# Kernel optimization log

Measured on AMD Instinct MI355X. Metric: run time of the kernel, lower is better.

## Reference

```python
import jax, jax.numpy as jnp
import numpy as np

B, C, IMG, P, D, L, NH, DFF = 8, 2, 256, 16, 1024, 8, 16, 4096
HP = IMG // P          # 16 patches per side
N = HP * HP            # 256 patch tokens
S = N + 1              # + cls token
HD = D // NH           # 64 head dim


def _ln(x, w, b, eps=1e-5):
    mu = x.mean(-1, keepdims=True)
    var = ((x - mu) ** 2).mean(-1, keepdims=True)
    return (x - mu) * jax.lax.rsqrt(var + eps) * w + b


def _decay_mask():
    # RetNetRelPos2d(D, NH, initial_value=1, heads_range=NH): per-head log-decay
    decay = jnp.log(1.0 - 2.0 ** (-1.0 - NH * jnp.arange(NH, dtype=jnp.float32) / NH))
    idx = jnp.arange(HP)
    gy, gx = jnp.meshgrid(idx, idx, indexing='ij')
    grid = jnp.stack([gy.ravel(), gx.ravel()], -1)                 # [N,2]
    dist = jnp.abs(grid[:, None] - grid[None, :]).sum(-1)          # [N,N] Manhattan
    mask = decay[:, None, None] * dist.astype(jnp.float32)        # [NH,N,N]
    return jnp.pad(mask, ((0, 0), (1, 0), (1, 0)))                 # cls: zero decay


def setup_inputs() -> dict:
    key = jax.random.key(0)
    ks = iter(jax.random.split(key, 16))
    g = lambda shape: jax.random.normal(next(ks), shape, jnp.float32) * 0.02
    return dict(
        imgs=jax.random.normal(next(ks), (B, C, IMG, IMG), jnp.float32),
        patch_w=g((C, P, P, D)), patch_b=jnp.zeros((D,), jnp.float32),
        cls_tok=g((1, 1, D)),
        ln1_w=jnp.ones((L, D), jnp.float32), ln1_b=jnp.zeros((L, D), jnp.float32),
        wq=g((L, D, D)), wk=g((L, D, D)), wv=g((L, D, D)),
        bq=jnp.zeros((L, D), jnp.float32), bk=jnp.zeros((L, D), jnp.float32), bv=jnp.zeros((L, D), jnp.float32),
        wo=g((L, D, D)), bo=jnp.zeros((L, D), jnp.float32),
        ln2_w=jnp.ones((L, D), jnp.float32), ln2_b=jnp.zeros((L, D), jnp.float32),
        w1=g((L, D, DFF)), b1=jnp.zeros((L, DFF), jnp.float32),
        w2=g((L, DFF, D)), b2=jnp.zeros((L, D), jnp.float32),
        normf_w=jnp.ones((D,), jnp.float32), normf_b=jnp.zeros((D,), jnp.float32),
        enpred_w=g((D, P * P * 2)), enpred_b=jnp.zeros((P * P * 2,), jnp.float32),
    )


def reference(imgs, patch_w, patch_b, cls_tok, ln1_w, ln1_b, wq, wk, wv, bq, bk, bv,
              wo, bo, ln2_w, ln2_b, w1, b1, w2, b2, normf_w, normf_b, enpred_w, enpred_b):
    b = imgs.shape[0]
    # PatchEmbed: conv with stride==kernel == patch extraction + linear
    xp = imgs.reshape(b, C, HP, P, HP, P)
    x = jnp.einsum('nchpwq,cpqd->nhwd', xp, patch_w).reshape(b, N, D) + patch_b
    residual = x
    x = jnp.concatenate([jnp.broadcast_to(cls_tok, (b, 1, D)), x], axis=1)  # [b,S,D]
    mask = _decay_mask()  # [NH,S,S]
    scale = HD ** -0.5
    for i in range(L):  # RMT blocks: pre-LN MaSA (softmax(qk*scale + decay)) + pre-LN GELU MLP
        h = _ln(x, ln1_w[i], ln1_b[i])
        q = (h @ wq[i] + bq[i]).reshape(b, S, NH, HD)
        k = (h @ wk[i] + bk[i]).reshape(b, S, NH, HD)
        v = (h @ wv[i] + bv[i]).reshape(b, S, NH, HD)
        logits = jnp.einsum('bqhd,bkhd->bhqk', q, k) * scale + mask
        attn = jax.nn.softmax(logits, axis=-1)
        o = jnp.einsum('bhqk,bkhd->bqhd', attn, v).reshape(b, S, D)
        x = x + o @ wo[i] + bo[i]
        h = _ln(x, ln2_w[i], ln2_b[i])
        x = x + jax.nn.gelu(h @ w1[i] + b1[i], approximate=False) @ w2[i] + b2[i]
    x = _ln(x, normf_w, normf_b)
    # PGSA on patch tokens as [b,D,HP,HP]
    t = x[:, 1:, :].transpose(0, 2, 1).reshape(b, D, HP, HP)
    n = HP * HP - 1
    mu = t.mean(axis=(2, 3), keepdims=True)
    xm2 = (t - mu) ** 2
    y = xm2 / (4.0 * (xm2.sum(axis=(2, 3), keepdims=True) / n + 1e-4)) + 0.5
    t = t * jax.nn.sigmoid(y)
    tokens = t.reshape(b, D, N).transpose(0, 2, 1) + residual
    pred = tokens @ enpred_w + enpred_b  # [b,N,P*P*2]
    # unpatchify -> [b,2,IMG,IMG]
    u = pred.reshape(b, HP, HP, P, P, 2)
    return jnp.einsum('nhwpqc->nchpwq', u).reshape(b, 2, IMG, IMG)
```

## Files before the change

kernel.cpp:

```cpp
#include <hip/hip_runtime.h>
#include <cstdint>
#include <cstddef>

#define BB    8
#define CCH   2
#define IMGD  256
#define PDIM  16
#define DD    1024
#define LLAY  8
#define NHEAD 16
#define DFFD  4096
#define NTOK  256
#define SD    257
#define HDD   64
#define MTOK  (BB*SD)
#define MPAT  (BB*NTOK)
#define MPAD  2176
#define KPAD  288

typedef unsigned short u16;
typedef __bf16 bf16x8 __attribute__((ext_vector_type(8)));
typedef float  f32x4  __attribute__((ext_vector_type(4)));

__device__ __forceinline__ u16 f2bf(float f) {
    uint32_t u = __float_as_uint(f);
    u += 0x7FFF + ((u >> 16) & 1);
    return (u16)(u >> 16);
}
__device__ __forceinline__ int imin(int a, int b) { return a < b ? a : b; }

#define GLB(p)  ((const __attribute__((address_space(1))) void*)(uintptr_t)(p))
#define LDSP(p) ((__attribute__((address_space(3))) void*)(uint32_t)(uintptr_t)(p))

template<int ACT, int OBF>
__global__ __launch_bounds__(256) void gemm128(
    const u16* __restrict__ A, const u16* __restrict__ BT,
    const float* __restrict__ bias, const float* __restrict__ Cin,
    void* __restrict__ Cout, int M, int N, int K)
{
    __shared__ u16 lds[8192];
    const int tid = threadIdx.x, wid = tid >> 6, lane = tid & 63;
    const int m0 = blockIdx.y * 128, n0 = blockIdx.x * 128;
    const int wm = (wid >> 1) * 64, wn = (wid & 1) * 64;
    const int srow = lane >> 2, scol = (lane & 3) * 8;
    const int l15 = lane & 15, loct = lane >> 4;

    f32x4 acc[4][4] = {};

    const size_t arow = (size_t)(m0 + wid * 16 + srow) * K + scol;
    const size_t brow = (size_t)(n0 + wid * 16 + srow) * K + scol;
    u16* ldsA = lds + wid * 512;
    u16* ldsB = lds + 4096 + wid * 512;

    for (int k0 = 0; k0 < K; k0 += 32) {
        __builtin_amdgcn_global_load_lds(GLB(A  + arow + k0),                 LDSP(ldsA),        16, 0, 0);
        __builtin_amdgcn_global_load_lds(GLB(A  + arow + (size_t)64*K + k0),  LDSP(ldsA + 2048), 16, 0, 0);
        __builtin_amdgcn_global_load_lds(GLB(BT + brow + k0),                 LDSP(ldsB),        16, 0, 0);
        __builtin_amdgcn_global_load_lds(GLB(BT + brow + (size_t)64*K + k0),  LDSP(ldsB + 2048), 16, 0, 0);
        __syncthreads();
        bf16x8 af[4], bfr[4];
        #pragma unroll
        for (int i = 0; i < 4; ++i)
            af[i] = *(const bf16x8*)(lds + (wm + i * 16 + l15) * 32 + loct * 8);
        #pragma unroll
        for (int j = 0; j < 4; ++j)
            bfr[j] = *(const bf16x8*)(lds + 4096 + (wn + j * 16 + l15) * 32 + loct * 8);
        #pragma unroll
        for (int i = 0; i < 4; ++i)
            #pragma unroll
            for (int j = 0; j < 4; ++j)
                acc[i][j] = __builtin_amdgcn_mfma_f32_16x16x32_bf16(af[i], bfr[j], acc[i][j], 0, 0, 0);
        __syncthreads();
    }

    #pragma unroll
    for (int j = 0; j < 4; ++j) {
        const int col = n0 + wn + j * 16 + l15;
        const float bv = bias[col];
        #pragma unroll
        for (int i = 0; i < 4; ++i) {
            const int rbase = m0 + wm + i * 16 + loct * 4;
            #pragma unroll
            for (int r = 0; r < 4; ++r) {
                const int row = rbase + r;
                if (row < M) {
                    float v = acc[i][j][r] + bv;
                    if (ACT) v = 0.5f * v * (1.f + erff(v * 0.70710678118654752f));
                    if (Cin) v += Cin[(size_t)row * N + col];
                    if (OBF) ((u16*)Cout)[(size_t)row * N + col] = f2bf(v);
                    else     ((float*)Cout)[(size_t)row * N + col] = v;
                }
            }
        }
    }
}

__global__ __launch_bounds__(256) void gemm_qkv(
    const u16* __restrict__ A, const u16* __restrict__ BT,
    const float* __restrict__ bias,
    u16* __restrict__ QKb, u16* __restrict__ VTg, int M, int K)
{
    __shared__ u16 lds[8192];
    const int tid = threadIdx.x, wid = tid >> 6, lane = tid & 63;
    const int m0 = blockIdx.y * 128, n0 = blockIdx.x * 128;
    const int wm = (wid >> 1) * 64, wn = (wid & 1) * 64;
    const int srow = lane >> 2, scol = (lane & 3) * 8;
    const int l15 = lane & 15, loct = lane >> 4;

    f32x4 acc[4][4] = {};
    const size_t arow = (size_t)(m0 + wid * 16 + srow) * K + scol;
    const size_t brow = (size_t)(n0 + wid * 16 + srow) * K + scol;
    u16* ldsA = lds + wid * 512;
    u16* ldsB = lds + 4096 + wid * 512;

    for (int k0 = 0; k0 < K; k0 += 32) {
        __builtin_amdgcn_global_load_lds(GLB(A  + arow + k0),                 LDSP(ldsA),        16, 0, 0);
        __builtin_amdgcn_global_load_lds(GLB(A  + arow + (size_t)64*K + k0),  LDSP(ldsA + 2048), 16, 0, 0);
        __builtin_amdgcn_global_load_lds(GLB(BT + brow + k0),                 LDSP(ldsB),        16, 0, 0);
        __builtin_amdgcn_global_load_lds(GLB(BT + brow + (size_t)64*K + k0),  LDSP(ldsB + 2048), 16, 0, 0);
        __syncthreads();
        bf16x8 af[4], bfr[4];
        #pragma unroll
        for (int i = 0; i < 4; ++i)
            af[i] = *(const bf16x8*)(lds + (wm + i * 16 + l15) * 32 + loct * 8);
        #pragma unroll
        for (int j = 0; j < 4; ++j)
            bfr[j] = *(const bf16x8*)(lds + 4096 + (wn + j * 16 + l15) * 32 + loct * 8);
        #pragma unroll
        for (int i = 0; i < 4; ++i)
            #pragma unroll
            for (int j = 0; j < 4; ++j)
                acc[i][j] = __builtin_amdgcn_mfma_f32_16x16x32_bf16(af[i], bfr[j], acc[i][j], 0, 0, 0);
        __syncthreads();
    }

    #pragma unroll
    for (int j = 0; j < 4; ++j) {
        const int col = n0 + wn + j * 16 + l15;
        const float bv = bias[col];
        #pragma unroll
        for (int i = 0; i < 4; ++i) {
            const int rbase = m0 + wm + i * 16 + loct * 4;
            #pragma unroll
            for (int r = 0; r < 4; ++r) {
                const int row = rbase + r;
                if (row < M) {
                    const float v = acc[i][j][r] + bv;
                    if (col < 2048) {
                        QKb[(size_t)row * 2048 + col] = f2bf(v);
                    } else {
                        const int b = row / SD;
                        const int key = row - b * SD;
                        VTg[((size_t)b * 1024 + (col - 2048)) * KPAD + key] = f2bf(v);
                    }
                }
            }
        }
    }
}

template<int ACT, int OBF>
__global__ __launch_bounds__(256) void gemm64(
    const u16* __restrict__ A, const u16* __restrict__ BT,
    const float* __restrict__ bias, const float* __restrict__ Cin,
    void* __restrict__ Cout, int M, int N, int K)
{
    __shared__ u16 lds[8192];
    const int tid = threadIdx.x, wid = tid >> 6, lane = tid & 63;
    const int m0 = blockIdx.y * 64, n0 = blockIdx.x * 64;
    const int wm = (wid >> 1) * 32, wn = (wid & 1) * 32;
    const int srow = lane >> 2, scol = (lane & 3) * 8;
    const int l15 = lane & 15, loct = lane >> 4;

    f32x4 acc[2][2] = {};
    const size_t arow = (size_t)(m0 + wid * 16 + srow) * K + scol;
    const size_t brow = (size_t)(n0 + wid * 16 + srow) * K + scol;
    u16* ldsA = lds + wid * 512;
    u16* ldsB = lds + 4096 + wid * 512;

    for (int k0 = 0; k0 < K; k0 += 64) {
        __builtin_amdgcn_global_load_lds(GLB(A  + arow + k0),      LDSP(ldsA),        16, 0, 0);
        __builtin_amdgcn_global_load_lds(GLB(A  + arow + k0 + 32), LDSP(ldsA + 2048), 16, 0, 0);
        __builtin_amdgcn_global_load_lds(GLB(BT + brow + k0),      LDSP(ldsB),        16, 0, 0);
        __builtin_amdgcn_global_load_lds(GLB(BT + brow + k0 + 32), LDSP(ldsB + 2048), 16, 0, 0);
        __syncthreads();
        #pragma unroll
        for (int t = 0; t < 2; ++t) {
            bf16x8 af[2], bfr[2];
            #pragma unroll
            for (int i = 0; i < 2; ++i)
                af[i] = *(const bf16x8*)(lds + t * 2048 + (wm + i * 16 + l15) * 32 + loct * 8);
            #pragma unroll
            for (int j = 0; j < 2; ++j)
                bfr[j] = *(const bf16x8*)(lds + 4096 + t * 2048 + (wn + j * 16 + l15) * 32 + loct * 8);
            #pragma unroll
            for (int i = 0; i < 2; ++i)
                #pragma unroll
                for (int j = 0; j < 2; ++j)
                    acc[i][j] = __builtin_amdgcn_mfma_f32_16x16x32_bf16(af[i], bfr[j], acc[i][j], 0, 0, 0);
        }
        __syncthreads();
    }

    #pragma unroll
    for (int j = 0; j < 2; ++j) {
        const int col = n0 + wn + j * 16 + l15;
        const float bv = bias[col];
        #pragma unroll
        for (int i = 0; i < 2; ++i) {
            const int rbase = m0 + wm + i * 16 + loct * 4;
            #pragma unroll
            for (int r = 0; r < 4; ++r) {
                const int row = rbase + r;
                if (row < M) {
                    float v = acc[i][j][r] + bv;
                    if (ACT) v = 0.5f * v * (1.f + erff(v * 0.70710678118654752f));
                    if (Cin) v += Cin[(size_t)row * N + col];
                    if (OBF) ((u16*)Cout)[(size_t)row * N + col] = f2bf(v);
                    else     ((float*)Cout)[(size_t)row * N + col] = v;
                }
            }
        }
    }
}

__global__ __launch_bounds__(256) void attn_fused(
    const u16* __restrict__ QKb, const u16* __restrict__ VTg,
    u16* __restrict__ O)
{
    __shared__ u16 P[4][16][296];
    const int tid = threadIdx.x, wid = tid >> 6, lane = tid & 63;
    const int l15 = lane & 15, loct = lane >> 4;
    const int bh = blockIdx.x, b = bh >> 4, h = bh & 15;
    const int q0 = blockIdx.y * 64 + wid * 16;

    const size_t qkbase = (size_t)b * SD * 2048 + h * 64;
    const u16* qp = QKb + qkbase + (size_t)imin(q0 + l15, SD - 1) * 2048;
    const bf16x8 qf0 = *(const bf16x8*)(qp + loct * 8);
    const bf16x8 qf1 = *(const bf16x8*)(qp + 32 + loct * 8);

    f32x4 s[17];
    #pragma unroll
    for (int nt = 0; nt < 17; ++nt) {
        const u16* kp = QKb + qkbase + (size_t)imin(nt * 16 + l15, SD - 1) * 2048 + 1024;
        const bf16x8 kf0 = *(const bf16x8*)(kp + loct * 8);
        const bf16x8 kf1 = *(const bf16x8*)(kp + 32 + loct * 8);
        f32x4 a = {};
        a = __builtin_amdgcn_mfma_f32_16x16x32_bf16(qf0, kf0, a, 0, 0, 0);
        a = __builtin_amdgcn_mfma_f32_16x16x32_bf16(qf1, kf1, a, 0, 0, 0);
        s[nt] = a;
    }

    const float dec = logf(1.f - exp2f(-1.f - (float)h));
    const int qb = q0 + loct * 4;
    float rmax[4] = {-3.4e38f, -3.4e38f, -3.4e38f, -3.4e38f};
    #pragma unroll
    for (int nt = 0; nt < 17; ++nt) {
        const int key = nt * 16 + l15;
        #pragma unroll
        for (int r = 0; r < 4; ++r) {
            float v;
            if (key >= SD) {
                v = -1e30f;
            } else {
                v = s[nt][r] * 0.125f;
                const int q = qb + r;
                if (q > 0 && key > 0) {
                    const int nq = q - 1, nk = key - 1;
                    const int dist = abs((nq >> 4) - (nk >> 4)) + abs((nq & 15) - (nk & 15));
                    v += dec * (float)dist;
                }
            }
            s[nt][r] = v;
            rmax[r] = fmaxf(rmax[r], v);
        }
    }
    #pragma unroll
    for (int r = 0; r < 4; ++r) {
        #pragma unroll
        for (int m = 1; m < 16; m <<= 1) rmax[r] = fmaxf(rmax[r], __shfl_xor(rmax[r], m));
    }
    float rsum[4] = {0.f, 0.f, 0.f, 0.f};
    #pragma unroll
    for (int nt = 0; nt < 17; ++nt)
        #pragma unroll
        for (int r = 0; r < 4; ++r) {
            const float e = __expf(s[nt][r] - rmax[r]);
            s[nt][r] = e;
            rsum[r] += e;
        }
    #pragma unroll
    for (int r = 0; r < 4; ++r) {
        #pragma unroll
        for (int m = 1; m < 16; m <<= 1) rsum[r] += __shfl_xor(rsum[r], m);
        rsum[r] = 1.f / rsum[r];
    }
    #pragma unroll
    for (int nt = 0; nt < 17; ++nt)
        #pragma unroll
        for (int r = 0; r < 4; ++r)
            P[wid][loct * 4 + r][nt * 16 + l15] = f2bf(s[nt][r] * rsum[r]);
    {
        const int rr = lane >> 2, cc = (lane & 3) * 4;
        #pragma unroll
        for (int i = 0; i < 4; ++i) P[wid][rr][272 + cc + i] = 0;
    }

    f32x4 o[4] = {};
    const u16* vrow = VTg + ((size_t)b * 1024 + h * 64) * KPAD;
    #pragma unroll
    for (int ks = 0; ks < 9; ++ks) {
        const bf16x8 pf = *(const bf16x8*)&P[wid][l15][ks * 32 + loct * 8];
        #pragma unroll
        for (int j = 0; j < 4; ++j) {
            const bf16x8 vf = *(const bf16x8*)(vrow + (size_t)(j * 16 + l15) * KPAD + ks * 32 + loct * 8);
            o[j] = __builtin_amdgcn_mfma_f32_16x16x32_bf16(pf, vf, o[j], 0, 0, 0);
        }
    }
    #pragma unroll
    for (int j = 0; j < 4; ++j)
        #pragma unroll
        for (int r = 0; r < 4; ++r) {
            const int q = qb + r;
            if (q < SD) O[((size_t)(b * SD + q)) * DD + h * 64 + j * 16 + l15] = f2bf(o[j][r]);
        }
}

__global__ __launch_bounds__(256) void transpose_bf16_k(
    const float* __restrict__ W, u16* __restrict__ WT, int K, int N)
{
    __shared__ float t[32][33];
    const int k0 = blockIdx.y * 32, n0 = blockIdx.x * 32;
    const int c = threadIdx.x & 31, rb = threadIdx.x >> 5;
    #pragma unroll
    for (int i = 0; i < 4; ++i) {
        const int r = rb + i * 8;
        t[r][c] = W[(size_t)(k0 + r) * N + n0 + c];
    }
    __syncthreads();
    #pragma unroll
    for (int i = 0; i < 4; ++i) {
        const int r = rb + i * 8;
        WT[(size_t)(n0 + r) * K + k0 + c] = f2bf(t[c][r]);
    }
}

__global__ __launch_bounds__(256) void cat3_k(const float* __restrict__ a,
                                              const float* __restrict__ b,
                                              const float* __restrict__ c,
                                              float* __restrict__ o)
{
    const int i = blockIdx.x * 256 + threadIdx.x;
    o[i] = (i < 1024) ? a[i] : (i < 2048 ? b[i - 1024] : c[i - 2048]);
}

__global__ __launch_bounds__(256) void im2col_k(const float* __restrict__ imgs,
                                                u16* __restrict__ Ao)
{
    const int idx = blockIdx.x * 256 + threadIdx.x;
    const int k = idx & 511, m = idx >> 9;
    const int b = m >> 8, n = m & 255;
    const int hp = n >> 4, wp = n & 15;
    const int c = k >> 8, p = (k >> 4) & 15, q = k & 15;
    Ao[idx] = f2bf(imgs[(((size_t)b * CCH + c) * IMGD + hp * PDIM + p) * IMGD + wp * PDIM + q]);
}

__global__ __launch_bounds__(256) void build_x_k(const float* __restrict__ RES,
                                                 const float* __restrict__ cls,
                                                 float* __restrict__ X)
{
    const int idx = blockIdx.x * 256 + threadIdx.x;
    const int d = idx & 1023;
    const int r = idx >> 10;
    const int b = r / SD;
    const int s = r - b * SD;
    X[idx] = (s == 0) ? cls[d] : RES[((size_t)(b * NTOK + s - 1)) * DD + d];
}

template<int OBF>
__global__ __launch_bounds__(256) void ln_rows(const float* __restrict__ X,
                                               const float* __restrict__ w,
                                               const float* __restrict__ bsrc,
                                               void* __restrict__ Y)
{
    const int row = blockIdx.x;
    const int tid = threadIdx.x;
    const float* xr = X + (size_t)row * DD;
    const float4 v = *(const float4*)(xr + tid * 4);
    float s  = v.x + v.y + v.z + v.w;
    float s2 = v.x * v.x + v.y * v.y + v.z * v.z + v.w * v.w;
    #pragma unroll
    for (int off = 1; off < 64; off <<= 1) {
        s  += __shfl_xor(s, off);
        s2 += __shfl_xor(s2, off);
    }
    __shared__ float rs[4], rs2[4];
    if ((tid & 63) == 0) { rs[tid >> 6] = s; rs2[tid >> 6] = s2; }
    __syncthreads();
    s  = rs[0] + rs[1] + rs[2] + rs[3];
    s2 = rs2[0] + rs2[1] + rs2[2] + rs2[3];
    const float mu  = s * (1.f / 1024.f);
    const float var = fmaf(-mu, mu, s2 * (1.f / 1024.f));
    const float ri  = rsqrtf(var + 1e-5f);
    const float4 wv = *(const float4*)(w + tid * 4);
    const float4 bv = *(const float4*)(bsrc + tid * 4);
    float4 o;
    o.x = (v.x - mu) * ri * wv.x + bv.x;
    o.y = (v.y - mu) * ri * wv.y + bv.y;
    o.z = (v.z - mu) * ri * wv.z + bv.z;
    o.w = (v.w - mu) * ri * wv.w + bv.w;
    if (OBF) {
        ushort4 o4 = make_ushort4(f2bf(o.x), f2bf(o.y), f2bf(o.z), f2bf(o.w));
        *(ushort4*)((u16*)Y + (size_t)row * DD + tid * 4) = o4;
    } else {
        *(float4*)((float*)Y + (size_t)row * DD + tid * 4) = o;
    }
}

__global__ __launch_bounds__(256) void pgsa_k(const float* __restrict__ Xf,
                                              const float* __restrict__ RES,
                                              u16* __restrict__ TOK)
{
    const int bd = blockIdx.x;
    const int b = bd >> 10, dch = bd & 1023;
    const int n = threadIdx.x;
    const float t = Xf[((size_t)(b * SD + 1 + n)) * DD + dch];
    __shared__ float red[4];
    float s = t;
    #pragma unroll
    for (int off = 1; off < 64; off <<= 1) s += __shfl_xor(s, off);
    if ((n & 63) == 0) red[n >> 6] = s;
    __syncthreads();
    const float mu = (red[0] + red[1] + red[2] + red[3]) * (1.f / 256.f);
    const float xm = t - mu;
    const float xm2 = xm * xm;
    __syncthreads();
    float s2 = xm2;
    #pragma unroll
    for (int off = 1; off < 64; off <<= 1) s2 += __shfl_xor(s2, off);
    if ((n & 63) == 0) red[n >> 6] = s2;
    __syncthreads();
    const float tot2 = red[0] + red[1] + red[2] + red[3];
    const float y = xm2 / (4.f * (tot2 * (1.f / 255.f) + 1e-4f)) + 0.5f;
    const float sig = 1.f / (1.f + expf(-y));
    const size_t ri = ((size_t)b * NTOK + n) * DD + dch;
    TOK[ri] = f2bf(fmaf(t, sig, RES[ri]));
}

__global__ __launch_bounds__(256) void unpatch_k(const float* __restrict__ PRED,
                                                 float* __restrict__ out)
{
    const int idx = blockIdx.x * 256 + threadIdx.x;
    const int j = idx & 255, i = (idx >> 8) & 255;
    const int c = (idx >> 16) & 1, b = idx >> 17;
    const int hp = i >> 4, p = i & 15, wp = j >> 4, q = j & 15;
    out[idx] = PRED[((size_t)b * NTOK + hp * 16 + wp) * 512 + (p * 16 + q) * 2 + c];
}

extern "C" void kernel_launch(void* const* d_in, const int* in_sizes, int n_in,
                              void* d_out, int out_size, void* d_ws, size_t ws_size,
                              hipStream_t stream)
{
    const float* imgs     = (const float*)d_in[0];
    const float* patch_w  = (const float*)d_in[1];
    const float* patch_b  = (const float*)d_in[2];
    const float* cls_tok  = (const float*)d_in[3];
    const float* ln1_w    = (const float*)d_in[4];
    const float* ln1_b    = (const float*)d_in[5];
    const float* wq       = (const float*)d_in[6];
    const float* wk       = (const float*)d_in[7];
    const float* wv       = (const float*)d_in[8];
    const float* bq       = (const float*)d_in[9];
    const float* bk       = (const float*)d_in[10];
    const float* bv       = (const float*)d_in[11];
    const float* wo       = (const float*)d_in[12];
    const float* bo       = (const float*)d_in[13];
    const float* ln2_w    = (const float*)d_in[14];
    const float* ln2_b    = (const float*)d_in[15];
    const float* w1       = (const float*)d_in[16];
    const float* b1       = (const float*)d_in[17];
    const float* w2       = (const float*)d_in[18];
    const float* b2       = (const float*)d_in[19];
    const float* normf_w  = (const float*)d_in[20];
    const float* normf_b  = (const float*)d_in[21];
    const float* enpred_w = (const float*)d_in[22];
    const float* enpred_b = (const float*)d_in[23];
    float* out = (float*)d_out;

    char* w = (char*)d_ws;
    float* X     = (float*)w;            w += (size_t)MTOK * DD * 4;
    float* RES   = (float*)w;            w += (size_t)MPAT * DD * 4;
    u16*   QKb   = (u16*)w;              w += (size_t)MPAD * 2048 * 2;
    u16*   VTg   = (u16*)w;              w += (size_t)BB * 1024 * KPAD * 2;
    char*  UNION = w;                    w += (size_t)MPAD * DFFD * 2;
    u16*   Hb    = (u16*)w;              w += (size_t)MPAD * DD * 2;
    u16*   Ob    = (u16*)w;              w += (size_t)MPAD * DD * 2;
    u16*   WT    = (u16*)w;              w += (size_t)DFFD * DD * 2;
    float* bias3 = (float*)w;            w += 3072 * 4;

    u16*   IM2b  = (u16*)UNION;
    u16*   GELUb = (u16*)UNION;
    float* PRED  = (float*)UNION;
    float* Hf    = (float*)QKb;
    u16*   TOKb  = Hb;

    hipMemsetAsync(VTg, 0, (size_t)BB * 1024 * KPAD * 2, stream);

    hipLaunchKernelGGL(im2col_k, dim3(4096), dim3(256), 0, stream, imgs, IM2b);
    hipLaunchKernelGGL(transpose_bf16_k, dim3(DD / 32, 512 / 32), dim3(256), 0, stream,
                       patch_w, WT, 512, DD);
    hipLaunchKernelGGL((gemm64<0,0>), dim3(DD / 64, MPAT / 64), dim3(256), 0, stream,
                       IM2b, WT, patch_b, (const float*)nullptr, (void*)RES, MPAT, DD, 512);
    hipLaunchKernelGGL(build_x_k, dim3(MTOK * DD / 256), dim3(256), 0, stream, RES, cls_tok, X);

    for (int i = 0; i < LLAY; ++i) {
        const size_t wOff = (size_t)i * DD * DD;
        hipLaunchKernelGGL((ln_rows<1>), dim3(MTOK), dim3(256), 0, stream,
                           X, ln1_w + i * DD, ln1_b + i * DD, (void*)Hb);
        hipLaunchKernelGGL(transpose_bf16_k, dim3(32, 32), dim3(256), 0, stream,
                           wq + wOff, WT,                     DD, DD);
        hipLaunchKernelGGL(transpose_bf16_k, dim3(32, 32), dim3(256), 0, stream,
                           wk + wOff, WT + (size_t)1024 * DD, DD, DD);
        hipLaunchKernelGGL(transpose_bf16_k, dim3(32, 32), dim3(256), 0, stream,
                           wv + wOff, WT + (size_t)2048 * DD, DD, DD);
        hipLaunchKernelGGL(cat3_k, dim3(12), dim3(256), 0, stream,
                           bq + i * DD, bk + i * DD, bv + i * DD, bias3);
        hipLaunchKernelGGL(gemm_qkv, dim3(3072 / 128, 17), dim3(256), 0, stream,
                           Hb, WT, bias3, QKb, VTg, MTOK, DD);
        hipLaunchKernelGGL(attn_fused, dim3(BB * NHEAD, 5), dim3(256), 0, stream,
                           QKb, VTg, Ob);
        hipLaunchKernelGGL(transpose_bf16_k, dim3(32, 32), dim3(256), 0, stream,
                           wo + wOff, WT, DD, DD);
        hipLaunchKernelGGL((gemm64<0,0>), dim3(DD / 64, 33), dim3(256), 0, stream,
                           Ob, WT, bo + i * DD, X, (void*)X, MTOK, DD, DD);
        hipLaunchKernelGGL((ln_rows<1>), dim3(MTOK), dim3(256), 0, stream,
                           X, ln2_w + i * DD, ln2_b + i * DD, (void*)Hb);
        hipLaunchKernelGGL(transpose_bf16_k, dim3(DFFD / 32, DD / 32), dim3(256), 0, stream,
                           w1 + (size_t)i * DD * DFFD, WT, DD, DFFD);
        hipLaunchKernelGGL((gemm128<1,1>), dim3(DFFD / 128, 17), dim3(256), 0, stream,
                           Hb, WT, b1 + i * DFFD, (const float*)nullptr, (void*)GELUb, MTOK, DFFD, DD);
        hipLaunchKernelGGL(transpose_bf16_k, dim3(DD / 32, DFFD / 32), dim3(256), 0, stream,
                           w2 + (size_t)i * DFFD * DD, WT, DFFD, DD);
        hipLaunchKernelGGL((gemm64<0,0>), dim3(DD / 64, 33), dim3(256), 0, stream,
                           GELUb, WT, b2 + i * DD, X, (void*)X, MTOK, DD, DFFD);
    }

    hipLaunchKernelGGL((ln_rows<0>), dim3(MTOK), dim3(256), 0, stream, X, normf_w, normf_b, (void*)Hf);
    hipLaunchKernelGGL(pgsa_k, dim3(BB * DD), dim3(256), 0, stream, Hf, RES, TOKb);
    hipLaunchKernelGGL(transpose_bf16_k, dim3(512 / 32, DD / 32), dim3(256), 0, stream,
                       enpred_w, WT, DD, 512);
    hipLaunchKernelGGL((gemm64<0,0>), dim3(512 / 64, MPAT / 64), dim3(256), 0, stream,
                       TOKb, WT, enpred_b, (const float*)nullptr, (void*)PRED, MPAT, 512, DD);
    hipLaunchKernelGGL(unpatch_k, dim3(4096), dim3(256), 0, stream, PRED, out);
}
```

Baseline: 2.150 ms.

## Batch weight transposes up front, split-K atomic FFN2, fold QKV bias concat

Every layer's weights are transposed to bf16 in a few batched launches before the layer loop, into per-layer workspace buffers, instead of per-layer transposes inside the loop. The FFN down-projection now uses a 128x128 tile GEMM with 4-way split-K whose partial sums are added into the residual X with float atomics. The QKV GEMM reads the three bias vectors directly, which removes the concat kernel. This cuts launch count and gives the K=4096 GEMM more blocks, at the cost of a much larger workspace and non-deterministic atomic summation order.

After: 2.184 ms. No clear change (+1.6%).

```diff
diff --git a/kernel.cpp b/kernel.cpp
--- a/kernel.cpp
+++ b/kernel.cpp
@@ -95,10 +95,11 @@
     }
 }
 
-__global__ __launch_bounds__(256) void gemm_qkv(
+template<int SPLIT>
+__global__ __launch_bounds__(256) void gemm128_sk(
     const u16* __restrict__ A, const u16* __restrict__ BT,
-    const float* __restrict__ bias,
-    u16* __restrict__ QKb, u16* __restrict__ VTg, int M, int K)
+    const float* __restrict__ bias, float* __restrict__ C,
+    int M, int N, int K)
 {
     __shared__ u16 lds[8192];
     const int tid = threadIdx.x, wid = tid >> 6, lane = tid & 63;
@@ -106,6 +107,67 @@
     const int wm = (wid >> 1) * 64, wn = (wid & 1) * 64;
     const int srow = lane >> 2, scol = (lane & 3) * 8;
     const int l15 = lane & 15, loct = lane >> 4;
+    const int Ks = K / SPLIT;
+    const int kb = blockIdx.z * Ks;
+
+    f32x4 acc[4][4] = {};
+
+    const size_t arow = (size_t)(m0 + wid * 16 + srow) * K + scol + kb;
+    const size_t brow = (size_t)(n0 + wid * 16 + srow) * K + scol + kb;
+    u16* ldsA = lds + wid * 512;
+    u16* ldsB = lds + 4096 + wid * 512;
+
+    for (int k0 = 0; k0 < Ks; k0 += 32) {
+        __builtin_amdgcn_global_load_lds(GLB(A  + arow + k0),                 LDSP(ldsA),        16, 0, 0);
+        __builtin_amdgcn_global_load_lds(GLB(A  + arow + (size_t)64*K + k0),  LDSP(ldsA + 2048), 16, 0, 0);
+        __builtin_amdgcn_global_load_lds(GLB(BT + brow + k0),                 LDSP(ldsB),        16, 0, 0);
+        __builtin_amdgcn_global_load_lds(GLB(BT + brow + (size_t)64*K + k0),  LDSP(ldsB + 2048), 16, 0, 0);
+        __syncthreads();
+        bf16x8 af[4], bfr[4];
+        #pragma unroll
+        for (int i = 0; i < 4; ++i)
+            af[i] = *(const bf16x8*)(lds + (wm + i * 16 + l15) * 32 + loct * 8);
+        #pragma unroll
+        for (int j = 0; j < 4; ++j)
+            bfr[j] = *(const bf16x8*)(lds + 4096 + (wn + j * 16 + l15) * 32 + loct * 8);
+        #pragma unroll
+        for (int i = 0; i < 4; ++i)
+            #pragma unroll
+            for (int j = 0; j < 4; ++j)
+                acc[i][j] = __builtin_amdgcn_mfma_f32_16x16x32_bf16(af[i], bfr[j], acc[i][j], 0, 0, 0);
+        __syncthreads();
+    }
+
+    const int z0 = (blockIdx.z == 0);
+    #pragma unroll
+    for (int j = 0; j < 4; ++j) {
+        const int col = n0 + wn + j * 16 + l15;
+        const float bv = z0 ? bias[col] : 0.f;
+        #pragma unroll
+        for (int i = 0; i < 4; ++i) {
+            const int rbase = m0 + wm + i * 16 + loct * 4;
+            #pragma unroll
+            for (int r = 0; r < 4; ++r) {
+                const int row = rbase + r;
+                if (row < M)
+                    unsafeAtomicAdd(&C[(size_t)row * N + col], acc[i][j][r] + bv);
+            }
+        }
+    }
+}
+
+__global__ __launch_bounds__(256) void gemm_qkv(
+    const u16* __restrict__ A, const u16* __restrict__ BT,
+    const float* __restrict__ bq, const float* __restrict__ bk,
+    const float* __restrict__ bvp,
+    u16* __restrict__ QKb, u16* __restrict__ VTg, int M, int K)
+{
+    __shared__ u16 lds[8192];
+    const int tid = threadIdx.x, wid = tid >> 6, lane = tid & 63;
+    const int m0 = blockIdx.y * 128, n0 = blockIdx.x * 128;
+    const int wm = (wid >> 1) * 64, wn = (wid & 1) * 64;
+    const int srow = lane >> 2, scol = (lane & 3) * 8;
+    const int l15 = lane & 15, loct = lane >> 4;
 
     f32x4 acc[4][4] = {};
     const size_t arow = (size_t)(m0 + wid * 16 + srow) * K + scol;
@@ -137,7 +199,9 @@
     #pragma unroll
     for (int j = 0; j < 4; ++j) {
         const int col = n0 + wn + j * 16 + l15;
-        const float bv = bias[col];
+        const float bval = (col < 1024) ? bq[col]
+                         : (col < 2048) ? bk[col - 1024]
+                                        : bvp[col - 2048];
         #pragma unroll
         for (int i = 0; i < 4; ++i) {
             const int rbase = m0 + wm + i * 16 + loct * 4;
@@ -145,7 +209,7 @@
             for (int r = 0; r < 4; ++r) {
                 const int row = rbase + r;
                 if (row < M) {
-                    const float v = acc[i][j][r] + bv;
+                    const float v = acc[i][j][r] + bval;
                     if (col < 2048) {
                         QKb[(size_t)row * 2048 + col] = f2bf(v);
                     } else {
@@ -326,32 +390,26 @@
         }
 }
 
-__global__ __launch_bounds__(256) void transpose_bf16_k(
-    const float* __restrict__ W, u16* __restrict__ WT, int K, int N)
+__global__ __launch_bounds__(256) void transpose_bf16_b(
+    const float* __restrict__ W, u16* __restrict__ WT, int K, int N,
+    size_t sstrideZ, size_t dstrideZ)
 {
     __shared__ float t[32][33];
+    const float* Wz = W + (size_t)blockIdx.z * sstrideZ;
+    u16* WTz = WT + (size_t)blockIdx.z * dstrideZ;
     const int k0 = blockIdx.y * 32, n0 = blockIdx.x * 32;
     const int c = threadIdx.x & 31, rb = threadIdx.x >> 5;
     #pragma unroll
     for (int i = 0; i < 4; ++i) {
         const int r = rb + i * 8;
-        t[r][c] = W[(size_t)(k0 + r) * N + n0 + c];
+        t[r][c] = Wz[(size_t)(k0 + r) * N + n0 + c];
     }
     __syncthreads();
     #pragma unroll
     for (int i = 0; i < 4; ++i) {
         const int r = rb + i * 8;
-        WT[(size_t)(n0 + r) * K + k0 + c] = f2bf(t[c][r]);
-    }
-}
-
-__global__ __launch_bounds__(256) void cat3_k(const float* __restrict__ a,
-                                              const float* __restrict__ b,
-                                              const float* __restrict__ c,
-                                              float* __restrict__ o)
-{
-    const int i = blockIdx.x * 256 + threadIdx.x;
-    o[i] = (i < 1024) ? a[i] : (i < 2048 ? b[i - 1024] : c[i - 2048]);
+        WTz[(size_t)(n0 + r) * K + k0 + c] = f2bf(t[c][r]);
+    }
 }
 
 __global__ __launch_bounds__(256) void im2col_k(const float* __restrict__ imgs,
@@ -495,8 +553,12 @@
     char*  UNION = w;                    w += (size_t)MPAD * DFFD * 2;
     u16*   Hb    = (u16*)w;              w += (size_t)MPAD * DD * 2;
     u16*   Ob    = (u16*)w;              w += (size_t)MPAD * DD * 2;
-    u16*   WT    = (u16*)w;              w += (size_t)DFFD * DD * 2;
-    float* bias3 = (float*)w;            w += 3072 * 4;
+    u16*   WTqkv = (u16*)w;              w += (size_t)LLAY * 3072 * DD * 2;
+    u16*   WTwo  = (u16*)w;              w += (size_t)LLAY * DD * DD * 2;
+    u16*   WTw1  = (u16*)w;              w += (size_t)LLAY * DFFD * DD * 2;
+    u16*   WTw2  = (u16*)w;              w += (size_t)LLAY * DD * DFFD * 2;
+    u16*   WTpe  = (u16*)w;              w += (size_t)DD * 512 * 2;
+    u16*   WTen  = (u16*)w;              w += (size_t)512 * DD * 2;
 
     u16*   IM2b  = (u16*)UNION;
     u16*   GELUb = (u16*)UNION;
@@ -506,50 +568,50 @@
 
     hipMemsetAsync(VTg, 0, (size_t)BB * 1024 * KPAD * 2, stream);
 
+    hipLaunchKernelGGL(transpose_bf16_b, dim3(DD / 32, 512 / 32, 1), dim3(256), 0, stream,
+                       patch_w, WTpe, 512, DD, 0, 0);
+    hipLaunchKernelGGL(transpose_bf16_b, dim3(32, 32, LLAY), dim3(256), 0, stream,
+                       wq, WTqkv,                     DD, DD, (size_t)DD * DD, (size_t)3072 * DD);
+    hipLaunchKernelGGL(transpose_bf16_b, dim3(32, 32, LLAY), dim3(256), 0, stream,
+                       wk, WTqkv + (size_t)1024 * DD, DD, DD, (size_t)DD * DD, (size_t)3072 * DD);
+    hipLaunchKernelGGL(transpose_bf16_b, dim3(32, 32, LLAY), dim3(256), 0, stream,
+                       wv, WTqkv + (size_t)2048 * DD, DD, DD, (size_t)DD * DD, (size_t)3072 * DD);
+    hipLaunchKernelGGL(transpose_bf16_b, dim3(32, 32, LLAY), dim3(256), 0, stream,
+                       wo, WTwo, DD, DD, (size_t)DD * DD, (size_t)DD * DD);
+    hipLaunchKernelGGL(transpose_bf16_b, dim3(DFFD / 32, DD / 32, LLAY), dim3(256), 0, stream,
+                       w1, WTw1, DD, DFFD, (size_t)DD * DFFD, (size_t)DFFD * DD);
+    hipLaunchKernelGGL(transpose_bf16_b, dim3(DD / 32, DFFD / 32, LLAY), dim3(256), 0, stream,
+                       w2, WTw2, DFFD, DD, (size_t)DFFD * DD, (size_t)DD * DFFD);
+    hipLaunchKernelGGL(transpose_bf16_b, dim3(512 / 32, DD / 32, 1), dim3(256), 0, stream,
+                       enpred_w, WTen, DD, 512, 0, 0);
+
     hipLaunchKernelGGL(im2col_k, dim3(4096), dim3(256), 0, stream, imgs, IM2b);
-    hipLaunchKernelGGL(transpose_bf16_k, dim3(DD / 32, 512 / 32), dim3(256), 0, stream,
-                       patch_w, WT, 512, DD);
     hipLaunchKernelGGL((gemm64<0,0>), dim3(DD / 64, MPAT / 64), dim3(256), 0, stream,
-                       IM2b, WT, patch_b, (const float*)nullptr, (void*)RES, MPAT, DD, 512);
+                       IM2b, WTpe, patch_b, (const float*)nullptr, (void*)RES, MPAT, DD, 512);
     hipLaunchKernelGGL(build_x_k, dim3(MTOK * DD / 256), dim3(256), 0, stream, RES, cls_tok, X);
 
     for (int i = 0; i < LLAY; ++i) {
-        const size_t wOff = (size_t)i * DD * DD;
         hipLaunchKernelGGL((ln_rows<1>), dim3(MTOK), dim3(256), 0, stream,
                            X, ln1_w + i * DD, ln1_b + i * DD, (void*)Hb);
-        hipLaunchKernelGGL(transpose_bf16_k, dim3(32, 32), dim3(256), 0, stream,
-                           wq + wOff, WT,                     DD, DD);
-        hipLaunchKernelGGL(transpose_bf16_k, dim3(32, 32), dim3(256), 0, stream,
-                           wk + wOff, WT + (size_t)1024 * DD, DD, DD);
-        hipLaunchKernelGGL(transpose_bf16_k, dim3(32, 32), dim3(256), 0, stream,
-                           wv + wOff, WT + (size_t)2048 * DD, DD, DD);
-        hipLaunchKernelGGL(cat3_k, dim3(12), dim3(256), 0, stream,
-                           bq + i * DD, bk + i * DD, bv + i * DD, bias3);
         hipLaunchKernelGGL(gemm_qkv, dim3(3072 / 128, 17), dim3(256), 0, stream,
-                           Hb, WT, bias3, QKb, VTg, MTOK, DD);
+                           Hb, WTqkv + (size_t)i * 3072 * DD,
+                           bq + i * DD, bk + i * DD, bv + i * DD, QKb, VTg, MTOK, DD);
         hipLaunchKernelGGL(attn_fused, dim3(BB * NHEAD, 5), dim3(256), 0, stream,
                            QKb, VTg, Ob);
-        hipLaunchKernelGGL(transpose_bf16_k, dim3(32, 32), dim3(256), 0, stream,
-                           wo + wOff, WT, DD, DD);
         hipLaunchKernelGGL((gemm64<0,0>), dim3(DD / 64, 33), dim3(256), 0, stream,
-                           Ob, WT, bo + i * DD, X, (void*)X, MTOK, DD, DD);
+                           Ob, WTwo + (size_t)i * DD * DD, bo + i * DD, X, (void*)X, MTOK, DD, DD);
         hipLaunchKernelGGL((ln_rows<1>), dim3(MTOK), dim3(256), 0, stream,
                            X, ln2_w + i * DD, ln2_b + i * DD, (void*)Hb);
-        hipLaunchKernelGGL(transpose_bf16_k, dim3(DFFD / 32, DD / 32), dim3(256), 0, stream,
-                           w1 + (size_t)i * DD * DFFD, WT, DD, DFFD);
         hipLaunchKernelGGL((gemm128<1,1>), dim3(DFFD / 128, 17), dim3(256), 0, stream,
-                           Hb, WT, b1 + i * DFFD, (const float*)nullptr, (void*)GELUb, MTOK, DFFD, DD);
-        hipLaunchKernelGGL(transpose_bf16_k, dim3(DD / 32, DFFD / 32), dim3(256), 0, stream,
-                           w2 + (size_t)i * DFFD * DD, WT, DFFD, DD);
-        hipLaunchKernelGGL((gemm64<0,0>), dim3(DD / 64, 33), dim3(256), 0, stream,
-                           GELUb, WT, b2 + i * DD, X, (void*)X, MTOK, DD, DFFD);
+                           Hb, WTw1 + (size_t)i * DFFD * DD, b1 + i * DFFD,
+                           (const float*)nullptr, (void*)GELUb, MTOK, DFFD, DD);
+        hipLaunchKernelGGL((gemm128_sk<4>), dim3(DD / 128, 17, 4), dim3(256), 0, stream,
+                           GELUb, WTw2 + (size_t)i * DD * DFFD, b2 + i * DD, X, MTOK, DD, DFFD);
     }
 
     hipLaunchKernelGGL((ln_rows<0>), dim3(MTOK), dim3(256), 0, stream, X, normf_w, normf_b, (void*)Hf);
     hipLaunchKernelGGL(pgsa_k, dim3(BB * DD), dim3(256), 0, stream, Hf, RES, TOKb);
-    hipLaunchKernelGGL(transpose_bf16_k, dim3(512 / 32, DD / 32), dim3(256), 0, stream,
-                       enpred_w, WT, DD, 512);
     hipLaunchKernelGGL((gemm64<0,0>), dim3(512 / 64, MPAT / 64), dim3(256), 0, stream,
-                       TOKb, WT, enpred_b, (const float*)nullptr, (void*)PRED, MPAT, 512, DD);
+                       TOKb, WTen, enpred_b, (const float*)nullptr, (void*)PRED, MPAT, 512, DD);
     hipLaunchKernelGGL(unpatch_k, dim3(4096), dim3(256), 0, stream, PRED, out);
 }
```
